# Kernel tuning notes

Hardware: AMD Instinct MI355X
Metric: run time of the kernel (lower is better)

## Reference

```python
import jax, jax.numpy as jnp
import numpy as np
from jax.scipy.special import logsumexp

N, T, F, S, L = 16, 800, 90, 128, 200
NEG = -1e30
DEN_SCALE = 1.0


def setup_inputs() -> dict:
    key = jax.random.key(0)
    ks = jax.random.split(key, 6)
    # nnet_output is the output of log_softmax (per the docstring)
    logits = jax.random.normal(ks[0], (N, T, F), dtype=jnp.float32)
    nnet_output = jax.nn.log_softmax(logits, axis=-1)
    seq_idx = jnp.arange(N, dtype=jnp.int32)
    starts = jnp.zeros((N,), dtype=jnp.int32)
    nframes = jax.random.randint(ks[1], (N,), T // 2, T + 1).astype(jnp.int32)
    supervision_segments = jnp.stack([seq_idx, starts, nframes], axis=1)
    # shared denominator graph: dense log transition weights + state phone labels
    den_trans = jax.random.normal(ks[2], (S, S), dtype=jnp.float32) - 2.0
    den_labels = jax.random.randint(ks[3], (S,), 0, F).astype(jnp.int32)
    # numerator linear-chain graphs: per-utterance phone label sequences
    num_labels = jax.random.randint(ks[4], (N, L), 0, F).astype(jnp.int32)
    num_lens = jax.random.randint(ks[5], (N,), L // 2, L + 1).astype(jnp.int32)
    return {
        'nnet_output': nnet_output,
        'supervision_segments': supervision_segments,
        'den_trans': den_trans,
        'den_labels': den_labels,
        'num_labels': num_labels,
        'num_lens': num_lens,
    }


def _mmi_tot_scores(nnet_output, num_frames, den_trans, den_labels, num_labels, num_lens):
    """Log-semiring forward scores: num - den_scale * den per utterance."""
    x = jnp.transpose(nnet_output, (1, 0, 2))  # [T, N, F]
    ts = jnp.arange(T)

    # ---- denominator: shared dense WFSA, forward algorithm ----
    def den_step(alpha, inp):
        x_t, t = inp  # x_t: [N, F]
        emit = x_t[:, den_labels]  # [N, S] gather of frame log-probs
        new = logsumexp(alpha[:, :, None] + den_trans[None, :, :], axis=1) + emit
        alpha = jnp.where((t < num_frames)[:, None], new, alpha)
        return alpha, None

    a0 = jnp.full((N, S), NEG, dtype=nnet_output.dtype).at[:, 0].set(0.0)
    den_alpha, _ = jax.lax.scan(den_step, a0, (x, ts))
    den_scores = logsumexp(den_alpha, axis=1)  # [N]

    # ---- numerator: per-utterance linear chain (self-loop or advance) ----
    def num_step(alpha, inp):
        x_t, t = inp
        emit = jnp.take_along_axis(x_t, num_labels, axis=1)  # [N, L]
        body = jnp.logaddexp(alpha[:, 1:], alpha[:, :L]) + emit
        new = jnp.concatenate(
            [jnp.full((N, 1), NEG, dtype=alpha.dtype), body], axis=1)
        alpha = jnp.where((t < num_frames)[:, None], new, alpha)
        return alpha, None

    b0 = jnp.full((N, L + 1), NEG, dtype=nnet_output.dtype).at[:, 0].set(0.0)
    num_alpha, _ = jax.lax.scan(num_step, b0, (x, ts))
    num_scores = jnp.take_along_axis(num_alpha, num_lens[:, None], axis=1)[:, 0]

    return num_scores - DEN_SCALE * den_scores


def reference(nnet_output, supervision_segments, den_trans, den_labels, num_labels, num_lens):
    num_frames = supervision_segments[:, 2]
    tot = _mmi_tot_scores(nnet_output, num_frames, den_trans, den_labels,
                          num_labels, num_lens)
    # drop sequences whose score diverged (mirrors get_tot_objf_and_num_frames)
    finite = jnp.isfinite(tot) & (tot > 0.5 * NEG)
    tot_score = jnp.sum(jnp.where(finite, tot, 0.0))
    tot_frames = jnp.sum(jnp.where(finite, num_frames, 0))
    all_frames = jnp.sum(num_frames)
    return tot_score, tot_frames, all_frames
```

## Files before the change

kernel.cpp:

```cpp
#include <hip/hip_runtime.h>
#include <math.h>

#define NB 16
#define TT 800
#define FF 90
#define SS 128
#define LL 200
#define NEGV (-1e30f)

#define DNODES 16
#define DNDRX 50
#define QNODES 32
#define QDRX 25
#define BROW 26
#define BST 28
#define NEGH (-60000.0f)
#define EPAD 228
#define LN2F 0.69314718055994531f
#define LOG2E 1.4426950408889634f

typedef __attribute__((ext_vector_type(8))) short short8;
typedef __attribute__((ext_vector_type(4))) float float4v;
typedef _Float16 h4 __attribute__((ext_vector_type(4)));

static __device__ __forceinline__ unsigned short f2bf(float x) {
    union { float f; unsigned u; } v; v.f = x;
    unsigned r = (v.u + 0x7FFFu + ((v.u >> 16) & 1u)) >> 16;
    return (unsigned short)r;
}
static __device__ __forceinline__ unsigned packperm(float a, float b) {
    return __builtin_amdgcn_perm(__float_as_uint(b), __float_as_uint(a),
                                 0x07060302u);
}
static __device__ __forceinline__ int xsw(int row, int wrd) {
    return (wrd & 3) | ((((wrd >> 2) ^ (row & 7)) << 2));
}

__global__ __launch_bounds__(512, 2) void mmi_nodes(
    const float* __restrict__ x,
    const int*   __restrict__ sup,
    const float* __restrict__ trans,
    const int*   __restrict__ den_labels,
    const int*   __restrict__ num_labels,
    unsigned*    __restrict__ Pout,
    float*       __restrict__ scales8,
    _Float16*    __restrict__ Bd)
{
    __shared__ __align__(16) unsigned char SMEM[45632];
    const int tid = threadIdx.x;

    if (blockIdx.x < NB * DNODES) {
        const int bid = blockIdx.x;
        const int u  = bid >> 4;
        const int nd = bid & 15;
        const int t0 = nd * DNDRX;
        const int nf = sup[u * 3 + 2];
        unsigned* Pg = Pout + (size_t)bid * 8192;

        if (t0 >= nf) {
            #pragma unroll
            for (int k2 = 0; k2 < 16; ++k2) {
                const int ww = tid + k2 * 512;
                const int row = ww >> 6, colw = ww & 63;
                unsigned val = 0;
                if (row == 2 * colw)     val |= 0x3F80u;
                if (row == 2 * colw + 1) val |= 0x3F800000u;
                Pg[ww] = val;
            }
            if (tid < 8) scales8[bid * 8 + tid] = 0.0f;
            return;
        }

        const int w = tid >> 6, l = tid & 63;
        const int m15 = l & 15, q = l >> 4, h = m15 & 7;

        unsigned* AFs = (unsigned*)SMEM;
        #pragma unroll
        for (int i = 0; i < 16; ++i) {
            const int wi = tid + i * 512;
            const int f  = wi >> 2, j2 = wi & 3;
            const int fl = f & 63, kc = (f >> 6) & 3, mt = f >> 8;
            const int col = mt * 16 + (fl & 15);
            const int krow = kc * 32 + (fl >> 4) * 8 + 2 * j2;
            const float a = __expf(trans[(krow    ) * SS + col]);
            const float b = __expf(trans[(krow + 1) * SS + col]);
            AFs[wi] = (unsigned)f2bf(a) | ((unsigned)f2bf(b) << 16);
        }
        __syncthreads();
        short8 afrag[8][4];
        #pragma unroll
        for (int mt = 0; mt < 8; ++mt)
            #pragma unroll
            for (int kc = 0; kc < 4; ++kc)
                afrag[mt][kc] =
                    *(const short8*)(AFs + ((mt * 4 + kc) * 64 + l) * 4);
        __syncthreads();

        unsigned* Xs    = (unsigned*)SMEM;
        unsigned* ptabH = (unsigned*)(SMEM + 32768);

        for (int idx = tid; idx < DNDRX * 64; idx += 512) {
            const int k = idx >> 6, r = idx & 63;
            const int q2 = r >> 4, mtt = r & 15;
            const int pr = (mtt >> 1) * 8 + 2 * q2 + (mtt & 1);
            const int fr = min(t0 + k, TT - 1);
            const float* xr = x + ((size_t)u * TT + fr) * FF;
            const float ea = __expf(xr[den_labels[2 * pr]]);
            const float eb = __expf(xr[den_labels[2 * pr + 1]]);
            ptabH[idx] = (unsigned)f2bf(ea) | ((unsigned)f2bf(eb) << 16);
        }
        __syncthreads();

        unsigned* Xw = Xs + w * (16 * 64);
        {
            const unsigned pp = ptabH[((l & 7) >> 1) * 16 + (l >> 3) * 2 +
                                      (l & 1)];
            const float p0 = __uint_as_float(pp << 16);
            const float p1 = __uint_as_float(pp & 0xFFFF0000u);
            #pragma unroll
            for (int k2 = 0; k2 < 16; ++k2) {
                const int R = w * 16 + k2;
                const float2 t2 = ((const float2*)trans)[R * 64 + l];
                Xw[k2 * 64 + xsw(k2, l)] = packperm(__expf(t2.x) * p0,
                                                    __expf(t2.y) * p1);
            }
        }

        const unsigned short* XwH = (const unsigned short*)Xw;
        const int kmax = min(DNDRX, nf - t0);
        int eacc = 0;
        float redmax = 1.0f;

        for (int k = 1; k < kmax; ++k) {
            const bool dosc = ((k & 3) == 0);
            float sc = 1.0f;
            if (dosc) {
                const float mm = fmaxf(redmax, 1e-37f);
                const int e = (int)((__float_as_uint(mm) >> 23) & 255u);
                sc = __uint_as_float((unsigned)(254 - e) << 23);
                eacc += (e - 127);
            }

            short8 bf[4];
            #pragma unroll
            for (int kc = 0; kc < 4; ++kc)
                bf[kc] = *(const short8*)(XwH + m15 * 128 +
                                          8 * (((kc << 2) | q) ^ h));

            float4v acc[8];
            #pragma unroll
            for (int mt = 0; mt < 8; ++mt) {
                float4v z = {0.f, 0.f, 0.f, 0.f};
                acc[mt] = z;
            }
            __builtin_amdgcn_s_setprio(1);
            #pragma unroll
            for (int kc = 0; kc < 4; ++kc)
                #pragma unroll
                for (int mt = 0; mt < 8; ++mt)
                    acc[mt] = __builtin_amdgcn_mfma_f32_16x16x32_bf16(
                        afrag[mt][kc], bf[kc], acc[mt], 0, 0, 0);
            __builtin_amdgcn_s_setprio(0);

            const bool dmax = ((k & 3) == 3);
            float vmax = 0.0f;
            const unsigned* pcb = ptabH + k * 64 + q * 16;
            #pragma unroll
            for (int i = 0; i < 4; ++i) {
                const uint4 pu = *(const uint4*)(pcb + 4 * i);
                float f0 = __uint_as_float(pu.x << 16);
                float f1 = __uint_as_float(pu.x & 0xFFFF0000u);
                float f2 = __uint_as_float(pu.y << 16);
                float f3 = __uint_as_float(pu.y & 0xFFFF0000u);
                float f4 = __uint_as_float(pu.z << 16);
                float f5 = __uint_as_float(pu.z & 0xFFFF0000u);
                float f6 = __uint_as_float(pu.w << 16);
                float f7 = __uint_as_float(pu.w & 0xFFFF0000u);
                if (dosc) {
                    f0 *= sc; f1 *= sc; f2 *= sc; f3 *= sc;
                    f4 *= sc; f5 *= sc; f6 *= sc; f7 *= sc;
                }
                acc[2 * i][0] *= f0;
                acc[2 * i][1] *= f1;
                acc[2 * i][2] *= f2;
                acc[2 * i][3] *= f3;
                acc[2 * i + 1][0] *= f4;
                acc[2 * i + 1][1] *= f5;
                acc[2 * i + 1][2] *= f6;
                acc[2 * i + 1][3] *= f7;
                if (dmax) {
                    vmax = fmaxf(vmax,
                        fmaxf(fmaxf(acc[2 * i][0], acc[2 * i][1]),
                              fmaxf(acc[2 * i][2], acc[2 * i][3])));
                    vmax = fmaxf(vmax,
                        fmaxf(fmaxf(acc[2 * i + 1][0], acc[2 * i + 1][1]),
                              fmaxf(acc[2 * i + 1][2], acc[2 * i + 1][3])));
                }
            }
            if (dmax) {
                #pragma unroll
                for (int off = 32; off >= 1; off >>= 1)
                    vmax = fmaxf(vmax, __shfl_xor(vmax, off, 64));
                redmax = vmax;
            }

            #pragma unroll
            for (int mt = 0; mt < 8; ++mt) {
                uint2 pk;
                pk.x = packperm(acc[mt][0], acc[mt][1]);
                pk.y = packperm(acc[mt][2], acc[mt][3]);
                *(uint2*)(Xw + m15 * 64 +
                          4 * (((mt << 1) | (q >> 1)) ^ h) + 2 * (q & 1)) = pk;
            }
        }

        #pragma unroll
        for (int k2 = 0; k2 < 16; ++k2)
            Pg[(w * 16 + k2) * 64 + l] = Xw[k2 * 64 + xsw(k2, l)];
        if (l == 0) scales8[bid * 8 + w] = (float)eacc;
        return;
    }

    {
        float* est = (float*)(SMEM + 16);

        const int qb    = blockIdx.x - NB * DNODES;
        const int slot0 = qb * 2;
        const int u     = slot0 / QNODES;
        const int nd0   = slot0 - u * QNODES;
        const int nf    = sup[u * 3 + 2];
        const int* nlu  = num_labels + u * LL;

        for (int idx = tid; idx < 2 * QDRX * EPAD; idx += 512) {
            const int g   = idx / (QDRX * EPAD);
            const int rem = idx - g * (QDRX * EPAD);
            const int tt  = rem / EPAD;
            const int j   = rem - tt * EPAD;
            const int jj  = min(j, 199);
            const int fr  = min((nd0 + g) * QDRX + tt, TT - 1);
            est[idx] = x[((size_t)u * TT + fr) * FF + nlu[jj]] * LOG2E;
        }
        __syncthreads();

        const int g  = tid >> 8;
        const int c  = tid & 255;
        const int nd = nd0 + g;
        const int t0 = nd * QDRX;
        const int kmaxg = min(QDRX, max(nf - t0, 0));
        const float* eg = est + g * (QDRX * EPAD);

        float a[BROW];
        a[0] = 0.0f;
        #pragma unroll
        for (int d = 1; d < BROW; ++d) a[d] = NEGV;

        const float* etc = eg + (c - 1);
        for (int t = 0; t < kmaxg; ++t, etc += EPAD) {
            const int tc = t + 1;
            #pragma unroll
            for (int d = BROW - 1; d >= 1; --d) {
                if (d <= tc) {
                    const float e  = etc[d];
                    const float aa = a[d], bb = a[d - 1];
                    const float mx = fmaxf(aa, bb);
                    const float dd = fminf(aa, bb) - mx;
                    a[d] = e + mx +
                           __builtin_amdgcn_logf(
                               1.0f + __builtin_amdgcn_exp2f(dd));
                }
            }
            a[0] = (c == 0) ? NEGV : (etc[0] + a[0]);
        }

        if (c <= 200) {
            _Float16* Bg = Bd + (size_t)(slot0 + g) * 201 * BST;
            #pragma unroll
            for (int d = 0; d < BROW; ++d) {
                const int r = c + d;
                if (r <= 200) Bg[r * BST + d] = (_Float16)fmaxf(a[d], NEGH);
            }
            if (c < BROW - 1) {
                for (int kk = c + 1; kk < BROW; ++kk)
                    Bg[c * BST + kk] = (_Float16)NEGH;
            }
        }
    }
}

__global__ __launch_bounds__(256) void mmi_chain(
    const unsigned short* __restrict__ Pmat,
    const _Float16* __restrict__ Bd,
    const float* __restrict__ scales8,
    const int* __restrict__ num_lens,
    const int* __restrict__ sup,
    float* __restrict__ dsc,
    unsigned* __restrict__ ctr,
    float* __restrict__ out)
{
    __shared__ float sh_v[SS];
    __shared__ float sh_part[8 * SS];
    __shared__ float sh_red[2];
    __shared__ float ab[2][232];
    __shared__ int sfl;

    const int tid = threadIdx.x;

    if (blockIdx.x < NB) {
        const int u = blockIdx.x;
        const int gg = tid & 31, c = tid >> 5;
        const unsigned short* Pu = Pmat + (size_t)u * DNODES * 16384;

        if (tid < SS) sh_v[tid] = (tid == 0) ? 1.0f : 0.0f;
        int   e2acc = 0;
        float sscal = 0.0f;

        uint2 curm[16], nxt[16];
        #pragma unroll
        for (int j = 0; j < 16; ++j)
            curm[j] = *(const uint2*)(Pu + (16 * c + j) * SS + 4 * gg);
        __syncthreads();

        for (int i = 0; i < DNODES; ++i) {
            if (i + 1 < DNODES) {
                const unsigned short* Pn = Pu + (size_t)(i + 1) * 16384;
                #pragma unroll
                for (int j = 0; j < 16; ++j)
                    nxt[j] = *(const uint2*)(Pn + (16 * c + j) * SS + 4 * gg);
            }
            const float* s8 = scales8 + (size_t)(u * DNODES + i) * 8;
            float gmax = s8[0];
            #pragma unroll
            for (int g2 = 1; g2 < 8; ++g2) gmax = fmaxf(gmax, s8[g2]);
            const float fgr = __builtin_amdgcn_exp2f(s8[c] - gmax);
            sscal += gmax;

            const float4* av = (const float4*)(sh_v + 16 * c);
            float4 aa[4] = {av[0], av[1], av[2], av[3]};
            const float* as = (const float*)aa;
            float4 acc = make_float4(0.f, 0.f, 0.f, 0.f);
            #pragma unroll
            for (int j = 0; j < 16; ++j) {
                const float e0 = __uint_as_float(curm[j].x << 16);
                const float e1 = __uint_as_float(curm[j].x & 0xFFFF0000u);
                const float e2 = __uint_as_float(curm[j].y << 16);
                const float e3 = __uint_as_float(curm[j].y & 0xFFFF0000u);
                acc.x = fmaf(as[j], e0, acc.x);
                acc.y = fmaf(as[j], e1, acc.y);
                acc.z = fmaf(as[j], e2, acc.z);
                acc.w = fmaf(as[j], e3, acc.w);
            }
            acc.x *= fgr; acc.y *= fgr; acc.z *= fgr; acc.w *= fgr;
            *(float4*)(sh_part + c * SS + 4 * gg) = acc;
            __syncthreads();

            float v = 0.0f;
            if (tid < SS) {
                float y = 0.0f;
                #pragma unroll
                for (int cc = 0; cc < 8; ++cc) y += sh_part[cc * SS + tid];
                v = y;
                float m = v;
                #pragma unroll
                for (int off = 32; off >= 1; off >>= 1)
                    m = fmaxf(m, __shfl_xor(m, off, 64));
                if ((tid & 63) == 0) sh_red[tid >> 6] = m;
            }
            __syncthreads();
            if (tid < SS) {
                const float mm = fmaxf(fmaxf(sh_red[0], sh_red[1]), 1e-37f);
                const int e = (int)((__float_as_uint(mm) >> 23) & 255u);
                const float inv = __uint_as_float((unsigned)(254 - e) << 23);
                e2acc += (e - 127);
                sh_v[tid] = v * inv;
            }
            #pragma unroll
            for (int j = 0; j < 16; ++j) curm[j] = nxt[j];
            __syncthreads();
        }

        if (tid < SS) {
            float s = sh_v[tid];
            #pragma unroll
            for (int off = 32; off >= 1; off >>= 1)
                s += __shfl_xor(s, off, 64);
            if ((tid & 63) == 0) sh_red[tid >> 6] = s;
        }
        __syncthreads();
        if (tid == 0)
            atomicExch(&dsc[u], LN2F * ((float)e2acc + sscal) +
                                __logf(sh_red[0] + sh_red[1]));
    } else {
        const int u = blockIdx.x - NB;
        const _Float16* Bu = Bd + (size_t)u * QNODES * 201 * BST;
        const int r = tid;
        const bool act = (r < 201);

        if (r < 232) { ab[0][r] = NEGV; ab[1][r] = NEGV; }
        h4 nx1[7], nx2[7];
        float dv[BROW];
        if (act) {
            const h4* s0 = (const h4*)(Bu + (size_t)r * BST);
            #pragma unroll
            for (int t7 = 0; t7 < 7; ++t7) nx1[t7] = s0[t7];
            #pragma unroll
            for (int k = 0; k < BROW; ++k) dv[k] = (float)nx1[k >> 2][k & 3];
            const h4* s1 = (const h4*)(Bu + ((size_t)201 + r) * BST);
            #pragma unroll
            for (int t7 = 0; t7 < 7; ++t7) nx1[t7] = s1[t7];
        }
        __syncthreads();
        if (r == 0) ab[0][QDRX] = 0.0f;
        __syncthreads();

        int cur = 0;
        for (int nd = 0; nd < QNODES; ++nd) {
            if (nd + 2 < QNODES && act) {
                const h4* src = (const h4*)(Bu + ((size_t)(nd + 2) * 201 + r) * BST);
                #pragma unroll
                for (int t7 = 0; t7 < 7; ++t7) nx2[t7] = src[t7];
            }
            float anew = NEGV;
            if (act) {
                float tr[BROW];
                #pragma unroll
                for (int k = 0; k < BROW; ++k)
                    tr[k] = dv[k] + ab[cur][QDRX + r - k];
                float m = tr[0];
                #pragma unroll
                for (int k = 1; k < BROW; ++k) m = fmaxf(m, tr[k]);
                float s = 0.0f;
                #pragma unroll
                for (int k = 0; k < BROW; ++k)
                    s += __builtin_amdgcn_exp2f(tr[k] - m);
                anew = m + __builtin_amdgcn_logf(s);
            }
            if (act) ab[cur ^ 1][QDRX + r] = anew;
            cur ^= 1;
            __syncthreads();
            if (act) {
                #pragma unroll
                for (int k = 0; k < BROW; ++k) dv[k] = (float)nx1[k >> 2][k & 3];
                #pragma unroll
                for (int t7 = 0; t7 < 7; ++t7) nx1[t7] = nx2[t7];
            }
        }
        if (r == 0)
            atomicExch(&dsc[NB + u], ab[cur][QDRX + num_lens[u]] * LN2F);
    }

    __threadfence();
    if (tid == 0) sfl = ((atomicAdd(ctr, 1u) & 31u) == 31u);
    __syncthreads();
    if (!sfl) return;
    __threadfence();
    if (tid < 64) {
        float tot_score = 0.0f, tot_frames = 0.0f, all_frames = 0.0f;
        if (tid < NB) {
            const float d = atomicAdd(&dsc[tid], 0.0f);
            const float n = atomicAdd(&dsc[NB + tid], 0.0f);
            const float tot = n - d;
            const int nf = sup[tid * 3 + 2];
            const bool fin = isfinite(tot) && (tot > 0.5f * NEGV);
            tot_score  = fin ? tot : 0.0f;
            tot_frames = fin ? (float)nf : 0.0f;
            all_frames = (float)nf;
        }
        #pragma unroll
        for (int off = 32; off >= 1; off >>= 1) {
            tot_score  += __shfl_xor(tot_score, off, 64);
            tot_frames += __shfl_xor(tot_frames, off, 64);
            all_frames += __shfl_xor(all_frames, off, 64);
        }
        if (tid == 0) {
            out[0] = tot_score;
            out[1] = tot_frames;
            out[2] = all_frames;
        }
    }
}

__global__ void mmi_finalize(const float* __restrict__ sc,
                             const int* __restrict__ sup,
                             float* __restrict__ out)
{
    const int tid = threadIdx.x;
    float tot_score = 0.0f, tot_frames = 0.0f, all_frames = 0.0f;
    if (tid < NB) {
        const float tot = sc[NB + tid] - sc[tid];
        const int nf = sup[tid * 3 + 2];
        const bool fin = isfinite(tot) && (tot > 0.5f * NEGV);
        tot_score  = fin ? tot : 0.0f;
        tot_frames = fin ? (float)nf : 0.0f;
        all_frames = (float)nf;
    }
    #pragma unroll
    for (int off = 32; off >= 1; off >>= 1) {
        tot_score  += __shfl_xor(tot_score, off, 64);
        tot_frames += __shfl_xor(tot_frames, off, 64);
        all_frames += __shfl_xor(all_frames, off, 64);
    }
    if (tid == 0) {
        out[0] = tot_score;
        out[1] = tot_frames;
        out[2] = all_frames;
    }
}

#define XBF (16 * FF)
__global__ __launch_bounds__(256) void mmi_forward_fb(
    const float* __restrict__ x, const int* __restrict__ sup,
    const float* __restrict__ trans, const int* __restrict__ den_labels,
    const int* __restrict__ num_labels, const int* __restrict__ num_lens,
    float* __restrict__ ws)
{
    const int tid = threadIdx.x;
    if (blockIdx.x < NB) {
        __shared__ float sh_v[SS];
        __shared__ float sh_part[8 * SS];
        __shared__ float sh_red[4];
        __shared__ __align__(16) float xbuf[2][XBF];
        const int n = blockIdx.x, nf = sup[n * 3 + 2];
        const int g = tid & 31, c = tid >> 5;
        float4 e[16];
        #pragma unroll
        for (int j = 0; j < 16; ++j) {
            const float4 t4 = *(const float4*)(trans + (size_t)(16 * c + j) * SS + 4 * g);
            e[j] = make_float4(__expf(t4.x), __expf(t4.y), __expf(t4.z), __expf(t4.w));
        }
        const int lab = (tid < SS) ? den_labels[tid & (SS - 1)] : 0;
        const float* xb = x + (size_t)n * TT * FF;
        {
            const float4* s0 = (const float4*)xb;
            float4 p0 = s0[tid]; float4 p1; if (tid < 104) p1 = s0[256 + tid];
            float4* d0 = (float4*)xbuf[0];
            d0[tid] = p0; if (tid < 104) d0[256 + tid] = p1;
        }
        if (tid < SS) sh_v[tid] = (tid == 0) ? 1.0f : 0.0f;
        float logM = 0.0f, v = 0.0f, pe = 0.0f;
        float4 pf0, pf1;
        __syncthreads();
        for (int t = 0; t < nf; ++t) {
            const int b = t >> 4;
            if (tid < SS) pe = __expf(xbuf[b & 1][(t & 15) * FF + lab]);
            float4 aa[4];
            { const float4* av = (const float4*)(sh_v + 16 * c);
              aa[0] = av[0]; aa[1] = av[1]; aa[2] = av[2]; aa[3] = av[3]; }
            const float* as = (const float*)aa;
            float4 acc = make_float4(0.f, 0.f, 0.f, 0.f);
            #pragma unroll
            for (int j = 0; j < 16; ++j) {
                acc.x = fmaf(as[j], e[j].x, acc.x); acc.y = fmaf(as[j], e[j].y, acc.y);
                acc.z = fmaf(as[j], e[j].z, acc.z); acc.w = fmaf(as[j], e[j].w, acc.w);
            }
            *(float4*)(sh_part + c * SS + 4 * g) = acc;
            if ((t & 15) == 8) {
                const int tn = (b + 1) * 16;
                if (tn < nf) {
                    const float4* s = (const float4*)(xb + (size_t)tn * FF);
                    pf0 = s[tid]; if (tid < 104) pf1 = s[256 + tid];
                }
            }
            __syncthreads();
            const bool rs = ((t & 15) == 15);
            if (tid < SS) {
                float y = 0.0f;
                #pragma unroll
                for (int cc = 0; cc < 8; ++cc) y += sh_part[cc * SS + tid];
                v = y * pe;
                if (rs) {
                    float m = v;
                    #pragma unroll
                    for (int off = 32; off >= 1; off >>= 1)
                        m = fmaxf(m, __shfl_xor(m, off, 64));
                    if ((tid & 63) == 0) sh_red[tid >> 6] = m;
                }
            }
            if (rs) {
                const int tn = (b + 1) * 16;
                if (tn < nf) {
                    float4* dst = (float4*)xbuf[(b + 1) & 1];
                    dst[tid] = pf0; if (tid < 104) dst[256 + tid] = pf1;
                }
                __syncthreads();
                if (tid < SS) {
                    float mm = fmaxf(fmaxf(sh_red[0], sh_red[1]), 1e-37f);
                    v *= (1.0f / mm); logM += __logf(mm);
                }
            }
            if (tid < SS) sh_v[tid] = v;
            __syncthreads();
        }
        if (tid < SS) {
            float ssum = v;
            #pragma unroll
            for (int off = 32; off >= 1; off >>= 1) ssum += __shfl_xor(ssum, off, 64);
            if ((tid & 63) == 0) sh_red[2 + (tid >> 6)] = ssum;
        }
        __syncthreads();
        if (tid == 0) ws[n] = logM + __logf(sh_red[2] + sh_red[3]);
    } else {
        const int w = tid >> 6, l = tid & 63;
        const int n = (blockIdx.x - NB) * 4 + w;
        const int nf = sup[n * 3 + 2];
        const float* xb = x + (size_t)n * TT * FF;
        const int* nl = num_labels + n * LL;
        int li[4];
        #pragma unroll
        for (int k = 0; k < 4; ++k) li[k] = nl[min(4 * l + k, LL - 1)];
        float a4[4] = {NEGV, NEGV, NEGV, NEGV};
        float ea[4], eb[4];
        #pragma unroll
        for (int k = 0; k < 4; ++k) ea[k] = xb[li[k]];
        { const float* xr = xb + (size_t)min(1, nf - 1) * FF;
          #pragma unroll
          for (int k = 0; k < 4; ++k) eb[k] = xr[li[k]]; }
        auto step = [&](float (&ee)[4], int t) {
            float left = __shfl_up(a4[3], 1, 64);
            if (l == 0) left = (t == 0) ? 0.0f : NEGV;
            float prev = left;
            #pragma unroll
            for (int k = 0; k < 4; ++k) {
                const float a = a4[k], b = prev;
                const float mx = fmaxf(a, b), mn = fminf(a, b);
                const float nv = mx + __logf(1.0f + __expf(mn - mx)) + ee[k];
                prev = a4[k]; a4[k] = nv;
            }
            const int t2 = min(t + 2, nf - 1);
            const float* xr = xb + (size_t)t2 * FF;
            #pragma unroll
            for (int k = 0; k < 4; ++k) ee[k] = xr[li[k]];
        };
        int t = 0;
        while (t < nf) { step(ea, t); ++t; if (t >= nf) break; step(eb, t); ++t; }
        const int idx = num_lens[n] - 1;
        if ((idx >> 2) == l) {
            const int kk = idx & 3;
            float vv = (kk == 0) ? a4[0] : (kk == 1) ? a4[1] : (kk == 2) ? a4[2] : a4[3];
            ws[NB + n] = vv;
        }
    }
}

extern "C" void kernel_launch(void* const* d_in, const int* in_sizes, int n_in,
                              void* d_out, int out_size, void* d_ws, size_t ws_size,
                              hipStream_t stream) {
    const float* x          = (const float*)d_in[0];
    const int*   sup        = (const int*)d_in[1];
    const float* trans      = (const float*)d_in[2];
    const int*   den_labels = (const int*)d_in[3];
    const int*   num_labels = (const int*)d_in[4];
    const int*   num_lens   = (const int*)d_in[5];
    float* out = (float*)d_out;

    const size_t PBYTES = (size_t)NB * DNODES * 32768;
    const size_t BBYTES = (size_t)NB * QNODES * 201 * BST * 2;
    const size_t SCB    = (size_t)NB * DNODES * 8 * sizeof(float);
    const size_t SOFF   = PBYTES + BBYTES;
    const size_t DOFF   = SOFF + SCB;
    const size_t COFF   = DOFF + 256;
    const size_t NEEDED = COFF + 256;

    if (ws_size >= NEEDED) {
        unsigned*  Pout    = (unsigned*)d_ws;
        _Float16*  Bd      = (_Float16*)((char*)d_ws + PBYTES);
        float*     scales8 = (float*)((char*)d_ws + SOFF);
        float*     dsc     = (float*)((char*)d_ws + DOFF);
        unsigned*  ctr     = (unsigned*)((char*)d_ws + COFF);
        mmi_nodes<<<dim3(512), dim3(512), 0, stream>>>(
            x, sup, trans, den_labels, num_labels, Pout, scales8, Bd);
        mmi_chain<<<dim3(2 * NB), dim3(256), 0, stream>>>(
            (const unsigned short*)d_ws, Bd, scales8, num_lens, sup,
            dsc, ctr, out);
    } else {
        float* ws = (float*)d_ws;
        mmi_forward_fb<<<dim3(20), dim3(256), 0, stream>>>(
            x, sup, trans, den_labels, num_labels, num_lens, ws);
        mmi_finalize<<<dim3(1), dim3(64), 0, stream>>>(ws, sup, out);
    }
}
```

Baseline: 175.4 us.

## Keep denominator product in registers via 32x32 MFMA and permlane32 swaps

The denominator node kernel now uses 4 waves of 256 threads, each owning 32 rows, and runs 32x32x16 bf16 MFMAs. The running product stays in accumulator registers and is repacked into B operands with permlane32_swap, which removes the per-step LDS round trip of the old 16x16 path. Scale tracking drops from 8 to 4 per-wave groups to match, and the numerator blocks each process one slot with 256 threads instead of two. The cost is more register pressure from the f32x16 accumulators plus pack/swap instructions on the serial chain, and the grid grows to 768 smaller blocks.

```diff
diff --git a/kernel.cpp b/kernel.cpp
--- a/kernel.cpp
+++ b/kernel.cpp
@@ -20,8 +20,9 @@
 #define LOG2E 1.4426950408889634f
 
 typedef __attribute__((ext_vector_type(8))) short short8;
-typedef __attribute__((ext_vector_type(4))) float float4v;
+typedef __attribute__((ext_vector_type(16))) float f32x16;
 typedef _Float16 h4 __attribute__((ext_vector_type(4)));
+typedef unsigned uint2v __attribute__((ext_vector_type(2)));
 
 static __device__ __forceinline__ unsigned short f2bf(float x) {
     union { float f; unsigned u; } v; v.f = x;
@@ -32,18 +33,15 @@
     return __builtin_amdgcn_perm(__float_as_uint(b), __float_as_uint(a),
                                  0x07060302u);
 }
-static __device__ __forceinline__ int xsw(int row, int wrd) {
-    return (wrd & 3) | ((((wrd >> 2) ^ (row & 7)) << 2));
-}
-
-__global__ __launch_bounds__(512, 2) void mmi_nodes(
+
+__global__ __launch_bounds__(256, 2) void mmi_nodes(
     const float* __restrict__ x,
     const int*   __restrict__ sup,
     const float* __restrict__ trans,
     const int*   __restrict__ den_labels,
     const int*   __restrict__ num_labels,
     unsigned*    __restrict__ Pout,
-    float*       __restrict__ scales8,
+    float*       __restrict__ scales4,
     _Float16*    __restrict__ Bd)
 {
     __shared__ __align__(16) unsigned char SMEM[45632];
@@ -59,74 +57,74 @@
 
         if (t0 >= nf) {
             #pragma unroll
-            for (int k2 = 0; k2 < 16; ++k2) {
-                const int ww = tid + k2 * 512;
+            for (int k2 = 0; k2 < 32; ++k2) {
+                const int ww = tid + k2 * 256;
                 const int row = ww >> 6, colw = ww & 63;
                 unsigned val = 0;
                 if (row == 2 * colw)     val |= 0x3F80u;
                 if (row == 2 * colw + 1) val |= 0x3F800000u;
                 Pg[ww] = val;
             }
-            if (tid < 8) scales8[bid * 8 + tid] = 0.0f;
+            if (tid < 4) scales4[bid * 4 + tid] = 0.0f;
             return;
         }
 
         const int w = tid >> 6, l = tid & 63;
-        const int m15 = l & 15, q = l >> 4, h = m15 & 7;
-
-        unsigned* AFs = (unsigned*)SMEM;
-        #pragma unroll
-        for (int i = 0; i < 16; ++i) {
-            const int wi = tid + i * 512;
+        const int l31 = l & 31, h = l >> 5;
+        const int row = w * 32 + l31;
+
+        unsigned* AFs   = (unsigned*)SMEM;
+        unsigned* ptabP = (unsigned*)(SMEM + 32768);
+
+        #pragma unroll
+        for (int i = 0; i < 32; ++i) {
+            const int wi = tid + i * 256;
             const int f  = wi >> 2, j2 = wi & 3;
-            const int fl = f & 63, kc = (f >> 6) & 3, mt = f >> 8;
-            const int col = mt * 16 + (fl & 15);
-            const int krow = kc * 32 + (fl >> 4) * 8 + 2 * j2;
+            const int fl = f & 63, kc = (f >> 6) & 7, mt = f >> 9;
+            const int col = mt * 32 + (fl & 31);
+            const int krow = kc * 16 + (fl >> 5) * 8 + 2 * j2;
             const float a = __expf(trans[(krow    ) * SS + col]);
             const float b = __expf(trans[(krow + 1) * SS + col]);
             AFs[wi] = (unsigned)f2bf(a) | ((unsigned)f2bf(b) << 16);
         }
-        __syncthreads();
-        short8 afrag[8][4];
-        #pragma unroll
-        for (int mt = 0; mt < 8; ++mt)
-            #pragma unroll
-            for (int kc = 0; kc < 4; ++kc)
-                afrag[mt][kc] =
-                    *(const short8*)(AFs + ((mt * 4 + kc) * 64 + l) * 4);
-        __syncthreads();
-
-        unsigned* Xs    = (unsigned*)SMEM;
-        unsigned* ptabH = (unsigned*)(SMEM + 32768);
-
-        for (int idx = tid; idx < DNDRX * 64; idx += 512) {
-            const int k = idx >> 6, r = idx & 63;
-            const int q2 = r >> 4, mtt = r & 15;
-            const int pr = (mtt >> 1) * 8 + 2 * q2 + (mtt & 1);
+        for (int idx = tid; idx < DNDRX * 64; idx += 256) {
+            const int k = idx >> 6, within = idx & 63;
+            const int h2 = within >> 5, rem = within & 31;
+            const int mt = rem >> 3, r2 = (rem >> 1) & 3, b = rem & 1;
+            const int cp = 16 * mt + 4 * r2 + 2 * h2 + b;
             const int fr = min(t0 + k, TT - 1);
             const float* xr = x + ((size_t)u * TT + fr) * FF;
-            const float ea = __expf(xr[den_labels[2 * pr]]);
-            const float eb = __expf(xr[den_labels[2 * pr + 1]]);
-            ptabH[idx] = (unsigned)f2bf(ea) | ((unsigned)f2bf(eb) << 16);
-        }
-        __syncthreads();
-
-        unsigned* Xw = Xs + w * (16 * 64);
-        {
-            const unsigned pp = ptabH[((l & 7) >> 1) * 16 + (l >> 3) * 2 +
-                                      (l & 1)];
-            const float p0 = __uint_as_float(pp << 16);
-            const float p1 = __uint_as_float(pp & 0xFFFF0000u);
-            #pragma unroll
-            for (int k2 = 0; k2 < 16; ++k2) {
-                const int R = w * 16 + k2;
-                const float2 t2 = ((const float2*)trans)[R * 64 + l];
-                Xw[k2 * 64 + xsw(k2, l)] = packperm(__expf(t2.x) * p0,
-                                                    __expf(t2.y) * p1);
-            }
-        }
-
-        const unsigned short* XwH = (const unsigned short*)Xw;
+            const float ea = __expf(xr[den_labels[2 * cp]]);
+            const float eb = __expf(xr[den_labels[2 * cp + 1]]);
+            ptabP[idx] = (unsigned)f2bf(ea) | ((unsigned)f2bf(eb) << 16);
+        }
+        __syncthreads();
+
+        short8 afrag[4][8];
+        #pragma unroll
+        for (int mt = 0; mt < 4; ++mt)
+            #pragma unroll
+            for (int kc = 0; kc < 8; ++kc)
+                afrag[mt][kc] =
+                    *(const short8*)(AFs + ((mt * 8 + kc) * 64 + l) * 4);
+
+        f32x16 acc[4];
+        #pragma unroll
+        for (int mt = 0; mt < 4; ++mt) {
+            #pragma unroll
+            for (int r2 = 0; r2 < 4; ++r2)
+                #pragma unroll
+                for (int b = 0; b < 2; ++b) {
+                    const float2 t2 = ((const float2*)(trans + (size_t)row * SS +
+                                        mt * 32 + 8 * r2 + 4 * h))[b];
+                    const unsigned pp = ptabP[h * 32 + mt * 8 + r2 * 2 + b];
+                    const float p0 = __uint_as_float(pp << 16);
+                    const float p1 = __uint_as_float(pp & 0xFFFF0000u);
+                    acc[mt][4 * r2 + 2 * b]     = __expf(t2.x) * p0;
+                    acc[mt][4 * r2 + 2 * b + 1] = __expf(t2.y) * p1;
+                }
+        }
+
         const int kmax = min(DNDRX, nf - t0);
         int eacc = 0;
         float redmax = 1.0f;
@@ -141,60 +139,57 @@
                 eacc += (e - 127);
             }
 
-            short8 bf[4];
-            #pragma unroll
-            for (int kc = 0; kc < 4; ++kc)
-                bf[kc] = *(const short8*)(XwH + m15 * 128 +
-                                          8 * (((kc << 2) | q) ^ h));
-
-            float4v acc[8];
-            #pragma unroll
-            for (int mt = 0; mt < 8; ++mt) {
-                float4v z = {0.f, 0.f, 0.f, 0.f};
+            unsigned pk[4][8];
+            #pragma unroll
+            for (int mt = 0; mt < 4; ++mt)
+                #pragma unroll
+                for (int p = 0; p < 8; ++p)
+                    pk[mt][p] = packperm(acc[mt][2 * p], acc[mt][2 * p + 1]);
+
+            #pragma unroll
+            for (int mt = 0; mt < 4; ++mt) {
+                f32x16 z = {0.f, 0.f, 0.f, 0.f, 0.f, 0.f, 0.f, 0.f,
+                            0.f, 0.f, 0.f, 0.f, 0.f, 0.f, 0.f, 0.f};
                 acc[mt] = z;
             }
-            __builtin_amdgcn_s_setprio(1);
-            #pragma unroll
-            for (int kc = 0; kc < 4; ++kc)
-                #pragma unroll
-                for (int mt = 0; mt < 8; ++mt)
-                    acc[mt] = __builtin_amdgcn_mfma_f32_16x16x32_bf16(
-                        afrag[mt][kc], bf[kc], acc[mt], 0, 0, 0);
-            __builtin_amdgcn_s_setprio(0);
+
+            #pragma unroll
+            for (int kc = 0; kc < 8; ++kc) {
+                const int s = kc & 1, mk = kc >> 1;
+                const uint2v s1 = __builtin_amdgcn_permlane32_swap(
+                    pk[mk][4 * s], pk[mk][4 * s + 2], false, false);
+                const uint2v s2 = __builtin_amdgcn_permlane32_swap(
+                    pk[mk][4 * s + 1], pk[mk][4 * s + 3], false, false);
+                union { unsigned u[4]; short8 s8; } B;
+                B.u[0] = s1[0]; B.u[1] = s2[0]; B.u[2] = s1[1]; B.u[3] = s2[1];
+                #pragma unroll
+                for (int mt = 0; mt < 4; ++mt)
+                    acc[mt] = __builtin_amdgcn_mfma_f32_32x32x16_bf16(
+                        afrag[mt][kc], B.s8, acc[mt], 0, 0, 0);
+            }
 
             const bool dmax = ((k & 3) == 3);
             float vmax = 0.0f;
-            const unsigned* pcb = ptabH + k * 64 + q * 16;
-            #pragma unroll
-            for (int i = 0; i < 4; ++i) {
-                const uint4 pu = *(const uint4*)(pcb + 4 * i);
-                float f0 = __uint_as_float(pu.x << 16);
-                float f1 = __uint_as_float(pu.x & 0xFFFF0000u);
-                float f2 = __uint_as_float(pu.y << 16);
-                float f3 = __uint_as_float(pu.y & 0xFFFF0000u);
-                float f4 = __uint_as_float(pu.z << 16);
-                float f5 = __uint_as_float(pu.z & 0xFFFF0000u);
-                float f6 = __uint_as_float(pu.w << 16);
-                float f7 = __uint_as_float(pu.w & 0xFFFF0000u);
-                if (dosc) {
-                    f0 *= sc; f1 *= sc; f2 *= sc; f3 *= sc;
-                    f4 *= sc; f5 *= sc; f6 *= sc; f7 *= sc;
-                }
-                acc[2 * i][0] *= f0;
-                acc[2 * i][1] *= f1;
-                acc[2 * i][2] *= f2;
-                acc[2 * i][3] *= f3;
-                acc[2 * i + 1][0] *= f4;
-                acc[2 * i + 1][1] *= f5;
-                acc[2 * i + 1][2] *= f6;
-                acc[2 * i + 1][3] *= f7;
-                if (dmax) {
-                    vmax = fmaxf(vmax,
-                        fmaxf(fmaxf(acc[2 * i][0], acc[2 * i][1]),
-                              fmaxf(acc[2 * i][2], acc[2 * i][3])));
-                    vmax = fmaxf(vmax,
-                        fmaxf(fmaxf(acc[2 * i + 1][0], acc[2 * i + 1][1]),
-                              fmaxf(acc[2 * i + 1][2], acc[2 * i + 1][3])));
+            const unsigned* pcb = ptabP + k * 64 + h * 32;
+            #pragma unroll
+            for (int mt = 0; mt < 4; ++mt) {
+                #pragma unroll
+                for (int half2 = 0; half2 < 2; ++half2) {
+                    const uint4 pu = *(const uint4*)(pcb + mt * 8 + 4 * half2);
+                    #pragma unroll
+                    for (int j = 0; j < 4; ++j) {
+                        const unsigned pw = (j == 0) ? pu.x : (j == 1) ? pu.y
+                                          : (j == 2) ? pu.z : pu.w;
+                        float f0 = __uint_as_float(pw << 16);
+                        float f1 = __uint_as_float(pw & 0xFFFF0000u);
+                        if (dosc) { f0 *= sc; f1 *= sc; }
+                        const int r0 = half2 * 8 + 2 * j;
+                        acc[mt][r0]     *= f0;
+                        acc[mt][r0 + 1] *= f1;
+                        if (dmax)
+                            vmax = fmaxf(vmax,
+                                fmaxf(acc[mt][r0], acc[mt][r0 + 1]));
+                    }
                 }
             }
             if (dmax) {
@@ -203,58 +198,54 @@
                     vmax = fmaxf(vmax, __shfl_xor(vmax, off, 64));
                 redmax = vmax;
             }
-
-            #pragma unroll
-            for (int mt = 0; mt < 8; ++mt) {
-                uint2 pk;
-                pk.x = packperm(acc[mt][0], acc[mt][1]);
-                pk.y = packperm(acc[mt][2], acc[mt][3]);
-                *(uint2*)(Xw + m15 * 64 +
-                          4 * (((mt << 1) | (q >> 1)) ^ h) + 2 * (q & 1)) = pk;
-            }
-        }
-
-        #pragma unroll
-        for (int k2 = 0; k2 < 16; ++k2)
-            Pg[(w * 16 + k2) * 64 + l] = Xw[k2 * 64 + xsw(k2, l)];
-        if (l == 0) scales8[bid * 8 + w] = (float)eacc;
+        }
+
+        unsigned* Xo = (unsigned*)SMEM;
+        #pragma unroll
+        for (int mt = 0; mt < 4; ++mt)
+            #pragma unroll
+            for (int p = 0; p < 8; ++p) {
+                const int cp = 16 * mt + 4 * (p >> 1) + 2 * h + (p & 1);
+                Xo[row * 64 + cp] = packperm(acc[mt][2 * p], acc[mt][2 * p + 1]);
+            }
+        __syncthreads();
+        #pragma unroll
+        for (int i = 0; i < 32; ++i) {
+            const int ww = tid + i * 256;
+            Pg[ww] = Xo[ww];
+        }
+        if (l == 0) scales4[bid * 4 + w] = (float)eacc;
         return;
     }
 
     {
-        float* est = (float*)(SMEM + 16);
-
-        const int qb    = blockIdx.x - NB * DNODES;
-        const int slot0 = qb * 2;
-        const int u     = slot0 / QNODES;
-        const int nd0   = slot0 - u * QNODES;
-        const int nf    = sup[u * 3 + 2];
-        const int* nlu  = num_labels + u * LL;
-
-        for (int idx = tid; idx < 2 * QDRX * EPAD; idx += 512) {
-            const int g   = idx / (QDRX * EPAD);
-            const int rem = idx - g * (QDRX * EPAD);
-            const int tt  = rem / EPAD;
-            const int j   = rem - tt * EPAD;
+        float* est = (float*)SMEM;
+
+        const int slot = blockIdx.x - NB * DNODES;
+        const int u    = slot >> 5;
+        const int nd   = slot & 31;
+        const int nf   = sup[u * 3 + 2];
+        const int* nlu = num_labels + u * LL;
+
+        for (int idx = tid; idx < QDRX * EPAD; idx += 256) {
+            const int tt  = idx / EPAD;
+            const int j   = idx - tt * EPAD;
             const int jj  = min(j, 199);
-            const int fr  = min((nd0 + g) * QDRX + tt, TT - 1);
+            const int fr  = min(nd * QDRX + tt, TT - 1);
             est[idx] = x[((size_t)u * TT + fr) * FF + nlu[jj]] * LOG2E;
         }
         __syncthreads();
 
-        const int g  = tid >> 8;
-        const int c  = tid & 255;
-        const int nd = nd0 + g;
+        const int c  = tid;
         const int t0 = nd * QDRX;
         const int kmaxg = min(QDRX, max(nf - t0, 0));
-        const float* eg = est + g * (QDRX * EPAD);
 
         float a[BROW];
         a[0] = 0.0f;
         #pragma unroll
         for (int d = 1; d < BROW; ++d) a[d] = NEGV;
 
-        const float* etc = eg + (c - 1);
+        const float* etc = est + (c - 1);
         for (int t = 0; t < kmaxg; ++t, etc += EPAD) {
             const int tc = t + 1;
             #pragma unroll
@@ -273,7 +264,7 @@
         }
 
         if (c <= 200) {
-            _Float16* Bg = Bd + (size_t)(slot0 + g) * 201 * BST;
+            _Float16* Bg = Bd + (size_t)slot * 201 * BST;
             #pragma unroll
             for (int d = 0; d < BROW; ++d) {
                 const int r = c + d;
@@ -290,7 +281,7 @@
 __global__ __launch_bounds__(256) void mmi_chain(
     const unsigned short* __restrict__ Pmat,
     const _Float16* __restrict__ Bd,
-    const float* __restrict__ scales8,
+    const float* __restrict__ scales4,
     const int* __restrict__ num_lens,
     const int* __restrict__ sup,
     float* __restrict__ dsc,
@@ -327,11 +318,9 @@
                 for (int j = 0; j < 16; ++j)
                     nxt[j] = *(const uint2*)(Pn + (16 * c + j) * SS + 4 * gg);
             }
-            const float* s8 = scales8 + (size_t)(u * DNODES + i) * 8;
-            float gmax = s8[0];
-            #pragma unroll
-            for (int g2 = 1; g2 < 8; ++g2) gmax = fmaxf(gmax, s8[g2]);
-            const float fgr = __builtin_amdgcn_exp2f(s8[c] - gmax);
+            const float* s4 = scales4 + (size_t)(u * DNODES + i) * 4;
+            const float gmax = fmaxf(fmaxf(s4[0], s4[1]), fmaxf(s4[2], s4[3]));
+            const float fgr = __builtin_amdgcn_exp2f(s4[c >> 1] - gmax);
             sscal += gmax;
 
             const float4* av = (const float4*)(sh_v + 16 * c);
@@ -654,7 +643,7 @@
 
     const size_t PBYTES = (size_t)NB * DNODES * 32768;
     const size_t BBYTES = (size_t)NB * QNODES * 201 * BST * 2;
-    const size_t SCB    = (size_t)NB * DNODES * 8 * sizeof(float);
+    const size_t SCB    = (size_t)NB * DNODES * 4 * sizeof(float);
     const size_t SOFF   = PBYTES + BBYTES;
     const size_t DOFF   = SOFF + SCB;
     const size_t COFF   = DOFF + 256;
@@ -663,13 +652,13 @@
     if (ws_size >= NEEDED) {
         unsigned*  Pout    = (unsigned*)d_ws;
         _Float16*  Bd      = (_Float16*)((char*)d_ws + PBYTES);
-        float*     scales8 = (float*)((char*)d_ws + SOFF);
+        float*     scales4 = (float*)((char*)d_ws + SOFF);
         float*     dsc     = (float*)((char*)d_ws + DOFF);
         unsigned*  ctr     = (unsigned*)((char*)d_ws + COFF);
-        mmi_nodes<<<dim3(512), dim3(512), 0, stream>>>(
-            x, sup, trans, den_labels, num_labels, Pout, scales8, Bd);
+        mmi_nodes<<<dim3(NB * DNODES + NB * QNODES), dim3(256), 0, stream>>>(
+            x, sup, trans, den_labels, num_labels, Pout, scales4, Bd);
         mmi_chain<<<dim3(2 * NB), dim3(256), 0, stream>>>(
-            (const unsigned short*)d_ws, Bd, scales8, num_lens, sup,
+            (const unsigned short*)d_ws, Bd, scales4, num_lens, sup,
             dsc, ctr, out);
     } else {
         float* ws = (float*)d_ws;
```

After: 167.6 us. 4.5% less time.
